# Kernel optimization log

Hardware: AMD Instinct MI355X
Metric: run time of the kernel (lower is better)

The kernel has to match this reference:

```python
import jax, jax.numpy as jnp
import numpy as np
import math

N = 100000
E = 1600000
D_IN = 128
H = 128
OUT = 10
NEG = -1e30


def setup_inputs() -> dict:
    key = jax.random.key(0)
    ks = jax.random.split(key, 24)
    def lin(k, fi, fo):
        s = 1.0 / np.sqrt(fi)
        return jax.random.uniform(k, (fi, fo), jnp.float32, -s, s)
    inp = {
        'x': jax.random.normal(ks[0], (N, D_IN), jnp.float32),
        'edge_index': jax.random.randint(ks[1], (2, E), 0, N, jnp.int64),
        'W1': lin(ks[2], D_IN, H), 'b1': jnp.zeros((H,), jnp.float32),
        'ws1': lin(ks[3], H, 1), 'bs1': jnp.zeros((1,), jnp.float32),
        'W2': lin(ks[4], H, H), 'b2': jnp.zeros((H,), jnp.float32),
        'ws2': lin(ks[5], H, 1), 'bs2': jnp.zeros((1,), jnp.float32),
        'W3': lin(ks[6], H, H), 'b3': jnp.zeros((H,), jnp.float32),
        'ws3': lin(ks[7], H, 1), 'bs3': jnp.zeros((1,), jnp.float32),
        'M1': lin(ks[8], 2 * H, H), 'bm1': jnp.zeros((H,), jnp.float32),
        'M2': lin(ks[9], H, H // 2), 'bm2': jnp.zeros((H // 2,), jnp.float32),
        'M3': lin(ks[10], H // 2, OUT), 'bm3': jnp.zeros((OUT,), jnp.float32),
    }
    return inp


def _gcn(x, W, b, src, dst, node_mask, edge_mask):
    # GCNConv with self-loops: deg[i] = self_loop + in_degree over valid edges
    deg = node_mask + jax.ops.segment_sum(edge_mask, dst, num_segments=N)
    dinv = jnp.where(deg > 0, jax.lax.rsqrt(deg), 0.0)
    coef = edge_mask * dinv[src] * dinv[dst]            # [E]
    agg = jax.ops.segment_sum(coef[:, None] * x[src], dst, num_segments=N)
    agg = agg + (node_mask * dinv * dinv)[:, None] * x   # self-loop term
    return (agg @ W + b) * node_mask[:, None]


def _sag_pool(x, ws, bs, src, dst, node_mask, edge_mask, k):
    # score via 1-dim GCNConv, top-k (ratio 0.5) select, tanh gating, edge filtering
    score = _gcn(x, ws, bs, src, dst, node_mask, edge_mask)[:, 0]
    _, idx = jax.lax.top_k(jnp.where(node_mask > 0, score, -jnp.inf), k)
    new_mask = jnp.zeros((N,), x.dtype).at[idx].set(1.0)
    x_new = x * jnp.tanh(score)[:, None] * new_mask[:, None]
    e_new = edge_mask * new_mask[src] * new_mask[dst]
    return x_new, new_mask, e_new


def _readout(x, mask, k):
    mean = jnp.sum(x * mask[:, None], axis=0) / k
    mx = jnp.max(jnp.where(mask[:, None] > 0, x, NEG), axis=0)
    return jnp.concatenate([mean, mx])[None, :]   # [1, 2H]


def reference(x, edge_index, W1, b1, ws1, bs1, W2, b2, ws2, bs2, W3, b3, ws3, bs3, M1, bm1, M2, bm2, M3, bm3):
    src, dst = edge_index[0], edge_index[1]
    nm0 = jnp.ones((N,), jnp.float32)
    em0 = jnp.ones((E,), jnp.float32)
    k1 = math.ceil(0.5 * N)
    k2 = math.ceil(0.5 * k1)
    k3 = math.ceil(0.5 * k2)

    h1 = jax.nn.relu(_gcn(x, W1, b1, src, dst, nm0, em0))
    x1, nm1, em1 = _sag_pool(h1, ws1, bs1, src, dst, nm0, em0, k1)
    r1 = _readout(x1, nm1, k1)

    h2 = jax.nn.relu(_gcn(x1, W2, b2, src, dst, nm1, em1))
    x2, nm2, em2 = _sag_pool(h2, ws2, bs2, src, dst, nm1, em1, k2)
    r2 = _readout(x2, nm2, k2)

    h3 = jax.nn.relu(_gcn(x2, W3, b3, src, dst, nm2, em2))
    x3, nm3, em3 = _sag_pool(h3, ws3, bs3, src, dst, nm2, em2, k3)
    r3 = _readout(x3, nm3, k3)

    readout = r1 + r2 + r3                              # [1, 2H]
    y = jax.nn.relu(readout @ M1 + bm1)
    y = jax.nn.relu(y @ M2 + bm2)
    y = y @ M3 + bm3
    return jax.nn.log_softmax(y, axis=1)
```

## Files before the change

### kernel.cpp

```cpp
#include <hip/hip_runtime.h>
#include <cstdint>
#include <cstddef>

#define NN 100000
#define EE 1600000
#define HH 128
#define NB_N 391
#define NBKT 391
#define CAP 5120


static __device__ __forceinline__ unsigned fsort_(float f){
  unsigned u = __float_as_uint(f);
  return (u & 0x80000000u) ? ~u : (u | 0x80000000u);
}
static __device__ __forceinline__ unsigned bfbits_(float f){
  unsigned u = __float_as_uint(f);
  return (u + 0x7FFFu + ((u >> 16) & 1u)) >> 16;
}
static __device__ __forceinline__ unsigned bfpack_(float f0, float f1){
  return bfbits_(f0) | (bfbits_(f1) << 16);
}
static __device__ __forceinline__ float bflo_(unsigned u){ return __uint_as_float(u << 16); }
static __device__ __forceinline__ float bfhi_(unsigned u){ return __uint_as_float(u & 0xFFFF0000u); }

__global__ void k_edgeflag(const int* __restrict__ ei, unsigned* __restrict__ state,
                           unsigned* __restrict__ bktcnt){
  int t = threadIdx.x;
  if(t < 64){
    int v = ei[2*t + 1];
    unsigned long long m = __ballot(v != 0);
    if(t == 0) state[8] = (m == 0ull) ? 1u : 0u;
  }
  if(t >= 12 && t < 24) state[t] = 0u;
  for(int j=t; j<NBKT; j+=256) bktcnt[j] = 0u;
}

__global__ __launch_bounds__(256) void k_binA(const int* __restrict__ ei,
                     const unsigned* __restrict__ state,
                     unsigned* __restrict__ bktcnt, unsigned* __restrict__ staging){
  __shared__ unsigned lcnt[NBKT];
  __shared__ unsigned lloc[NBKT];
  int t = threadIdx.x;
  for(int j=t; j<NBKT; j+=256){ lcnt[j] = 0u; lloc[j] = 0u; }
  bool i64 = (state[8] != 0u);
  int e0 = blockIdx.x*4096;
  int es[16], ed[16];
  #pragma unroll
  for(int k=0;k<16;k++){
    int e = e0 + k*256 + t;
    int s = -1, d = 0;
    if(e < EE){
      if(i64){ s = ei[2*e]; d = ei[2*EE + 2*e]; }
      else   { s = ei[e];   d = ei[EE + e]; }
    }
    es[k] = s; ed[k] = d;
  }
  __syncthreads();
  #pragma unroll
  for(int k=0;k<16;k++){
    if(es[k] >= 0) atomicAdd(&lcnt[ed[k]>>8], 1u);
  }
  __syncthreads();
  for(int j=t; j<NBKT; j+=256){
    unsigned c = lcnt[j];
    lcnt[j] = c ? atomicAdd(&bktcnt[j], c) : 0u;
  }
  __syncthreads();
  #pragma unroll
  for(int k=0;k<16;k++){
    if(es[k] >= 0){
      int b = ed[k] >> 8;
      unsigned off = lcnt[b] + atomicAdd(&lloc[b], 1u);
      if(off < CAP)
        staging[(unsigned)b*CAP + off] = (unsigned)es[k] | (((unsigned)(ed[k] & 255)) << 17);
    }
  }
}

__global__ __launch_bounds__(256) void k_binB(const unsigned* __restrict__ staging,
                     const unsigned* __restrict__ bktcnt,
                     int* __restrict__ rs, int* __restrict__ rl, int* __restrict__ col,
                     float* __restrict__ dinv){
  __shared__ unsigned hist[256];
  __shared__ unsigned pref[256];
  __shared__ unsigned lfill[256];
  __shared__ unsigned baseSh;
  int t = threadIdx.x;
  int b = blockIdx.x;
  unsigned s = 0;
  for(int j=t; j<b; j+=256) s += bktcnt[j];
  pref[t] = s;
  __syncthreads();
  for(int off=128; off>0; off>>=1){
    if(t < off) pref[t] += pref[t+off];
    __syncthreads();
  }
  if(t == 0) baseSh = pref[0];
  __syncthreads();
  unsigned base = baseSh;
  unsigned cnt = bktcnt[b]; if(cnt > CAP) cnt = CAP;
  hist[t] = 0u; lfill[t] = 0u;
  __syncthreads();
  const unsigned* st = staging + (unsigned)b*CAP;
  for(unsigned i=t; i<cnt; i+=256) atomicAdd(&hist[st[i]>>17], 1u);
  __syncthreads();
  unsigned h = hist[t];
  pref[t] = h;
  __syncthreads();
  for(int off=1; off<256; off<<=1){
    unsigned u = (t >= off) ? pref[t-off] : 0u;
    __syncthreads();
    pref[t] += u;
    __syncthreads();
  }
  unsigned excl = pref[t] - h;
  int node = b*256 + t;
  if(node < NN){
    rs[node] = (int)(base + excl);
    rl[node] = (int)h;
    dinv[node] = rsqrtf(1.f + (float)h);
  }
  __syncthreads();
  pref[t] = excl;
  __syncthreads();
  for(unsigned i=t; i<cnt; i+=256){
    unsigned w = st[i];
    unsigned dl = w >> 17;
    unsigned pos = base + pref[dl] + atomicAdd(&lfill[dl], 1u);
    col[pos] = (int)(w & 0x1FFFFu);
  }
}

template<int MODE>
__global__ __launch_bounds__(256) void k_gemm(const void* __restrict__ xin_,
        const float* __restrict__ gate, const int* __restrict__ alist, int nrows,
        const float* __restrict__ W, unsigned short* __restrict__ y16){
  __shared__ float sX[16][68];
  __shared__ float sW[16][64];
  __shared__ int rowid[64];
  __shared__ float rowg[64];
  int row0 = blockIdx.x*64, col0 = blockIdx.y*64;
  int t = threadIdx.x;
  if(t < 64){
    int gr = row0 + t;
    int node = -1; float gg = 0.f;
    if(gr < nrows){
      node = MODE ? alist[gr] : gr;
      gg = MODE ? gate[node] : 1.f;
    }
    rowid[t] = node; rowg[t] = gg;
  }
  __syncthreads();
  int tx = t & 15, ty = t >> 4;
  float acc[4][4] = {{0.f}};
  const float* xf = (const float*)xin_;
  const unsigned short* xh = (const unsigned short*)xin_;
  for(int kb=0; kb<HH; kb+=16){
    #pragma unroll
    for(int j=0;j<4;j++){
      int r = (t>>4) + j*16;
      int k = t & 15;
      int node = rowid[r];
      float v = 0.f;
      if(node >= 0){
        if(MODE) v = __uint_as_float(((unsigned)xh[(size_t)node*HH + kb + k]) << 16) * rowg[r];
        else     v = xf[(size_t)node*HH + kb + k];
      }
      sX[k][r] = v;
    }
    #pragma unroll
    for(int j=0;j<4;j++){
      int k = (t>>6) + j*4;
      int c = t & 63;
      sW[k][c] = W[(size_t)(kb+k)*HH + col0 + c];
    }
    __syncthreads();
    #pragma unroll
    for(int k=0;k<16;k++){
      float4 xv = *(const float4*)&sX[k][ty*4];
      float4 wv = *(const float4*)&sW[k][tx*4];
      float xs[4] = {xv.x, xv.y, xv.z, xv.w};
      float wsv[4] = {wv.x, wv.y, wv.z, wv.w};
      #pragma unroll
      for(int a=0;a<4;a++)
        #pragma unroll
        for(int b=0;b<4;b++)
          acc[a][b] += xs[a]*wsv[b];
    }
    __syncthreads();
  }
  #pragma unroll
  for(int a=0;a<4;a++){
    int node = rowid[ty*4 + a];
    if(node >= 0){
      uint2 o;
      o.x = bfpack_(acc[a][0], acc[a][1]);
      o.y = bfpack_(acc[a][2], acc[a][3]);
      *(uint2*)&y16[(size_t)node*HH + col0 + tx*4] = o;
    }
  }
}

template<int LIST>
__global__ __launch_bounds__(256) void k_agg(const unsigned short* __restrict__ y16,
        const float* __restrict__ dinv,
        const int* __restrict__ rs, const int* __restrict__ rl,
        const int* __restrict__ col, const int* __restrict__ alist,
        const float* __restrict__ bias, const float* __restrict__ wsc,
        unsigned short* __restrict__ h16, float* __restrict__ p,
        unsigned* __restrict__ hist){
  if(blockIdx.x < 512) hist[blockIdx.x*256 + threadIdx.x] = 0u;
  int w = (blockIdx.x*256 + threadIdx.x) >> 6;
  int lane = threadIdx.x & 63;
  int g = lane >> 4, c = lane & 15;
  int node = LIST ? alist[w] : w;
  float di = dinv[node];
  int e0 = rs[node], len = rl[node];
  float a0=0,a1=0,a2=0,a3=0,a4=0,a5=0,a6=0,a7=0;
  int i = g;
  for(; i + 4 < len; i += 8){
    int s0 = col[e0+i], s1 = col[e0+i+4];
    float d0 = dinv[s0], d1 = dinv[s1];
    uint4 v0 = ((const uint4*)(y16 + (size_t)s0*HH))[c];
    uint4 v1 = ((const uint4*)(y16 + (size_t)s1*HH))[c];
    a0 += d0*bflo_(v0.x) + d1*bflo_(v1.x);
    a1 += d0*bfhi_(v0.x) + d1*bfhi_(v1.x);
    a2 += d0*bflo_(v0.y) + d1*bflo_(v1.y);
    a3 += d0*bfhi_(v0.y) + d1*bfhi_(v1.y);
    a4 += d0*bflo_(v0.z) + d1*bflo_(v1.z);
    a5 += d0*bfhi_(v0.z) + d1*bfhi_(v1.z);
    a6 += d0*bflo_(v0.w) + d1*bflo_(v1.w);
    a7 += d0*bfhi_(v0.w) + d1*bfhi_(v1.w);
  }
  if(i < len){
    int s = col[e0+i];
    float ds = dinv[s];
    uint4 v = ((const uint4*)(y16 + (size_t)s*HH))[c];
    a0 += ds*bflo_(v.x); a1 += ds*bfhi_(v.x);
    a2 += ds*bflo_(v.y); a3 += ds*bfhi_(v.y);
    a4 += ds*bflo_(v.z); a5 += ds*bfhi_(v.z);
    a6 += ds*bflo_(v.w); a7 += ds*bfhi_(v.w);
  }
  a0 += __shfl_xor(a0,16,64); a0 += __shfl_xor(a0,32,64);
  a1 += __shfl_xor(a1,16,64); a1 += __shfl_xor(a1,32,64);
  a2 += __shfl_xor(a2,16,64); a2 += __shfl_xor(a2,32,64);
  a3 += __shfl_xor(a3,16,64); a3 += __shfl_xor(a3,32,64);
  a4 += __shfl_xor(a4,16,64); a4 += __shfl_xor(a4,32,64);
  a5 += __shfl_xor(a5,16,64); a5 += __shfl_xor(a5,32,64);
  a6 += __shfl_xor(a6,16,64); a6 += __shfl_xor(a6,32,64);
  a7 += __shfl_xor(a7,16,64); a7 += __shfl_xor(a7,32,64);
  uint4 sv = ((const uint4*)(y16 + (size_t)node*HH))[c];
  const float4* b4 = (const float4*)bias;
  float4 bb0 = b4[2*c], bb1 = b4[2*c+1];
  float d2 = di*di;
  float o0 = fmaxf(di*a0 + d2*bflo_(sv.x) + bb0.x, 0.f);
  float o1 = fmaxf(di*a1 + d2*bfhi_(sv.x) + bb0.y, 0.f);
  float o2 = fmaxf(di*a2 + d2*bflo_(sv.y) + bb0.z, 0.f);
  float o3 = fmaxf(di*a3 + d2*bfhi_(sv.y) + bb0.w, 0.f);
  float o4 = fmaxf(di*a4 + d2*bflo_(sv.z) + bb1.x, 0.f);
  float o5 = fmaxf(di*a5 + d2*bfhi_(sv.z) + bb1.y, 0.f);
  float o6 = fmaxf(di*a6 + d2*bflo_(sv.w) + bb1.z, 0.f);
  float o7 = fmaxf(di*a7 + d2*bfhi_(sv.w) + bb1.w, 0.f);
  if(g == 0){
    uint4 o;
    o.x = bfpack_(o0,o1); o.y = bfpack_(o2,o3);
    o.z = bfpack_(o4,o5); o.w = bfpack_(o6,o7);
    ((uint4*)(h16 + (size_t)node*HH))[c] = o;
  }
  const float4* w4 = (const float4*)wsc;
  float4 w0 = w4[2*c], w1 = w4[2*c+1];
  float pp = o0*w0.x + o1*w0.y + o2*w0.z + o3*w0.w
           + o4*w1.x + o5*w1.y + o6*w1.z + o7*w1.w;
  pp += __shfl_xor(pp, 1, 64);
  pp += __shfl_xor(pp, 2, 64);
  pp += __shfl_xor(pp, 4, 64);
  pp += __shfl_xor(pp, 8, 64);
  if(lane == 0) p[node] = pp;
}

template<int LIST>
__global__ void k_score(const float* __restrict__ p, const float* __restrict__ dinv,
                        const int* __restrict__ rs, const int* __restrict__ rl,
                        const int* __restrict__ col, const int* __restrict__ alist, int n,
                        const float* __restrict__ bs, float* __restrict__ score,
                        unsigned* __restrict__ key, unsigned* __restrict__ hist){
  int w = blockIdx.x*256 + threadIdx.x;
  if(w >= n) return;
  int i = LIST ? alist[w] : w;
  float di = dinv[i];
  float s = 0.f;
  int e0 = rs[i], len = rl[i];
  for(int e=e0; e<e0+len; e++){
    int cidx = col[e];
    s += dinv[cidx]*p[cidx];
  }
  float sc = di*s + di*di*p[i] + bs[0];
  score[i] = sc;
  unsigned kv = fsort_(sc);
  key[i] = kv;
  atomicAdd(&hist[kv>>16], 1u);
}

__global__ void k_hist_lo(const unsigned* __restrict__ key, const unsigned* __restrict__ state,
                          unsigned* __restrict__ histB){
  int i = blockIdx.x*256 + threadIdx.x;
  if(i < NN){
    unsigned kv = key[i];
    if((kv >> 16) == state[0]) atomicAdd(&histB[kv & 0xFFFFu], 1u);
  }
}
__global__ void k_pick(const unsigned* __restrict__ hist, unsigned* __restrict__ state,
                       int k_in, int mode){
  __shared__ unsigned csum[256];
  int t = threadIdx.x;
  const uint4* h4 = (const uint4*)(hist + t*256);
  unsigned s = 0;
  for(int j=0;j<64;j++){ uint4 v = h4[j]; s += v.x+v.y+v.z+v.w; }
  csum[t] = s;
  __syncthreads();
  for(int off=1; off<256; off<<=1){
    unsigned v = (t+off < 256) ? csum[t+off] : 0u;
    __syncthreads();
    csum[t] += v;
    __syncthreads();
  }
  unsigned k = (mode == 0) ? (unsigned)k_in : state[1];
  unsigned above = csum[t] - s;
  if(above < k && above + s >= k){
    unsigned run = above;
    for(int j=255; j>=0; j--){
      unsigned c = hist[t*256+j];
      if(run + c >= k){
        if(mode == 0){ state[0] = (unsigned)(t*256+j); state[1] = k - run; }
        else { state[2] = (state[0] << 16) | (unsigned)(t*256+j); state[3] = k - run; }
        break;
      }
      run += c;
    }
  }
}

__global__ __launch_bounds__(256) void k_maskCR(unsigned* __restrict__ key,
        const float* __restrict__ score, const unsigned* __restrict__ state,
        const unsigned short* __restrict__ h16,
        unsigned char* __restrict__ selm, float* __restrict__ gate,
        int* __restrict__ alist_out, unsigned* __restrict__ acounter,
        float* __restrict__ rpart, int slotbase){
  __shared__ int wcnt[4];
  __shared__ int priorSh;
  __shared__ int redi[256];
  __shared__ float gl[256];
  __shared__ unsigned char slf[256];
  __shared__ float4 red[256];
  __shared__ float out2[256];
  int t = threadIdx.x;
  int i = blockIdx.x*256 + t;
  unsigned T = state[2];
  int trem = (int)state[3];
  unsigned kv = (i < NN) ? key[i] : 0u;
  bool match = (kv == T);
  unsigned long long m = __ballot(match);
  int lane = t & 63, wid = t >> 6;
  if(lane == 0) wcnt[wid] = __popcll(m);
  if(t == 0) priorSh = 0;
  __syncthreads();
  int hasMatch = wcnt[0] | wcnt[1] | wcnt[2] | wcnt[3];
  int bbase = blockIdx.x*256;
  if(hasMatch){
    int cm = 0;
    for(int j = t*4; j < bbase; j += 1024){
      uint4 kk = *(const uint4*)&key[j];
      cm += (kk.x==T) + (kk.y==T) + (kk.z==T) + (kk.w==T);
    }
    redi[t] = cm;
    __syncthreads();
    for(int off=128; off>0; off>>=1){
      if(t < off) redi[t] += redi[t+off];
      __syncthreads();
    }
    if(t == 0) priorSh = redi[0];
    __syncthreads();
  }
  int pre = 0;
  for(int w=0; w<wid; w++) pre += wcnt[w];
  int lrank = __popcll(m & ((1ull << lane) - 1ull));
  int rank = priorSh + pre + lrank;
  bool sel = (kv > T) || (match && rank < trem);
  float gg = sel ? tanhf(score[i]) : 0.f;
  gl[t] = gg;
  slf[t] = sel ? 1 : 0;
  if(i < NN){
    selm[i] = sel ? 1 : 0;
    gate[i] = gg;
    if(!sel) key[i] = 0u;
  }
  unsigned long long sm = __ballot(sel);
  unsigned abase = 0;
  if(lane == 0) abase = atomicAdd(acounter, (unsigned)__popcll(sm));
  abase = (unsigned)__shfl((int)abase, 0, 64);
  if(sel) alist_out[abase + __popcll(sm & ((1ull << lane) - 1ull))] = i;
  __syncthreads();
  int ch = t & 15;
  int slot = t >> 4;
  float mm[8] = {0,0,0,0,0,0,0,0};
  float MM[8] = {-1e30f,-1e30f,-1e30f,-1e30f,-1e30f,-1e30f,-1e30f,-1e30f};
  for(int itr=0; itr<16; itr++){
    int nl = slot + itr*16;
    int node = bbase + nl;
    if(node < NN && slf[nl]){
      float g = gl[nl];
      uint4 v = ((const uint4*)(h16 + (size_t)node*HH))[ch];
      float x0 = g*bflo_(v.x), x1 = g*bfhi_(v.x);
      float x2 = g*bflo_(v.y), x3 = g*bfhi_(v.y);
      float x4 = g*bflo_(v.z), x5 = g*bfhi_(v.z);
      float x6 = g*bflo_(v.w), x7 = g*bfhi_(v.w);
      mm[0]+=x0; mm[1]+=x1; mm[2]+=x2; mm[3]+=x3;
      mm[4]+=x4; mm[5]+=x5; mm[6]+=x6; mm[7]+=x7;
      MM[0]=fmaxf(MM[0],x0); MM[1]=fmaxf(MM[1],x1); MM[2]=fmaxf(MM[2],x2); MM[3]=fmaxf(MM[3],x3);
      MM[4]=fmaxf(MM[4],x4); MM[5]=fmaxf(MM[5],x5); MM[6]=fmaxf(MM[6],x6); MM[7]=fmaxf(MM[7],x7);
    }
  }
  #pragma unroll
  for(int half=0; half<2; half++){
    red[t] = make_float4(mm[half*4+0],mm[half*4+1],mm[half*4+2],mm[half*4+3]);
    __syncthreads();
    if(t < 16){
      float4 sacc = red[t];
      for(int j=1;j<16;j++){
        float4 o = red[t + 16*j];
        sacc.x += o.x; sacc.y += o.y; sacc.z += o.z; sacc.w += o.w;
      }
      int d = t*8 + half*4;
      out2[d+0] = sacc.x; out2[d+1] = sacc.y; out2[d+2] = sacc.z; out2[d+3] = sacc.w;
    }
    __syncthreads();
    red[t] = make_float4(MM[half*4+0],MM[half*4+1],MM[half*4+2],MM[half*4+3]);
    __syncthreads();
    if(t < 16){
      float4 sacc = red[t];
      for(int j=1;j<16;j++){
        float4 o = red[t + 16*j];
        sacc.x = fmaxf(sacc.x,o.x); sacc.y = fmaxf(sacc.y,o.y);
        sacc.z = fmaxf(sacc.z,o.z); sacc.w = fmaxf(sacc.w,o.w);
      }
      int d = 128 + t*8 + half*4;
      out2[d+0] = sacc.x; out2[d+1] = sacc.y; out2[d+2] = sacc.z; out2[d+3] = sacc.w;
    }
    __syncthreads();
  }
  rpart[(size_t)(slotbase + blockIdx.x)*256 + t] = out2[t];
}

__global__ __launch_bounds__(256) void k_compact(const int* __restrict__ alist, int n,
        const unsigned char* __restrict__ selm,
        const int* __restrict__ rs_old, const int* __restrict__ rl_old,
        const int* __restrict__ col_old,
        int* __restrict__ rs_new, int* __restrict__ rl_new, int* __restrict__ col_new,
        float* __restrict__ dinv, unsigned* __restrict__ ecnt){
  __shared__ unsigned gcnt[16];
  __shared__ unsigned gbase[16];
  __shared__ unsigned blkbase;
  int t = threadIdx.x;
  int g = t >> 4, lane = t & 15;
  int gsh = ((t >> 4) & 3) * 16;
  int idx = blockIdx.x*16 + g;
  int node = -1, e0 = 0, len = 0;
  if(idx < n){ node = alist[idx]; e0 = rs_old[node]; len = rl_old[node]; }
  int cnt = 0;
  for(int i=lane; i<len; i+=16) cnt += selm[col_old[e0+i]];
  cnt += __shfl_xor(cnt,1,64); cnt += __shfl_xor(cnt,2,64);
  cnt += __shfl_xor(cnt,4,64); cnt += __shfl_xor(cnt,8,64);
  if(lane == 0) gcnt[g] = (node >= 0) ? (unsigned)cnt : 0u;
  __syncthreads();
  if(t == 0){
    unsigned s = 0;
    for(int j=0;j<16;j++){ gbase[j] = s; s += gcnt[j]; }
    blkbase = s ? atomicAdd(ecnt, s) : 0u;
  }
  __syncthreads();
  unsigned base = blkbase + gbase[g];
  if(node >= 0 && lane == 0){
    rs_new[node] = (int)base;
    rl_new[node] = cnt;
    dinv[node] = rsqrtf(1.f + (float)cnt);
  }
  int pos = (int)base;
  for(int i0=0; i0<len; i0+=16){
    int i = i0 + lane;
    bool keep = false; int s = 0;
    if(i < len){ s = col_old[e0+i]; keep = (selm[s] != 0); }
    unsigned long long b = __ballot(keep);
    unsigned gb = (unsigned)((b >> gsh) & 0xFFFFull);
    int rank = __popc(gb & ((1u << lane) - 1u));
    if(keep) col_new[pos + rank] = s;
    pos += __popc(gb);
  }
}

__global__ void k_mlp(const float* __restrict__ rpart,
                      const float* __restrict__ M1, const float* __restrict__ bm1,
                      const float* __restrict__ M2, const float* __restrict__ bm2,
                      const float* __restrict__ M3, const float* __restrict__ bm3,
                      float* __restrict__ out){
  __shared__ float R[256];
  __shared__ float y1[128];
  __shared__ float y2[64];
  __shared__ float y3[16];
  int t = threadIdx.x;
  const float kinv[3] = {1.f/50000.f, 1.f/25000.f, 1.f/12500.f};
  if(t < 128){
    float acc = 0.f;
    for(int l=0; l<3; l++){
      float s0=0.f,s1=0.f,s2=0.f,s3=0.f;
      int base = l*NB_N;
      int j = 0;
      for(; j+3 < NB_N; j += 4){
        s0 += rpart[(size_t)(base+j  )*256 + t];
        s1 += rpart[(size_t)(base+j+1)*256 + t];
        s2 += rpart[(size_t)(base+j+2)*256 + t];
        s3 += rpart[(size_t)(base+j+3)*256 + t];
      }
      for(; j < NB_N; j++) s0 += rpart[(size_t)(base+j)*256 + t];
      acc += ((s0+s1)+(s2+s3)) * kinv[l];
    }
    R[t] = acc;
  } else {
    float acc = 0.f;
    for(int l=0; l<3; l++){
      float m0=-1e30f,m1=-1e30f,m2=-1e30f,m3=-1e30f;
      int base = l*NB_N;
      int j = 0;
      for(; j+3 < NB_N; j += 4){
        m0 = fmaxf(m0, rpart[(size_t)(base+j  )*256 + t]);
        m1 = fmaxf(m1, rpart[(size_t)(base+j+1)*256 + t]);
        m2 = fmaxf(m2, rpart[(size_t)(base+j+2)*256 + t]);
        m3 = fmaxf(m3, rpart[(size_t)(base+j+3)*256 + t]);
      }
      for(; j < NB_N; j++) m0 = fmaxf(m0, rpart[(size_t)(base+j)*256 + t]);
      acc += fmaxf(fmaxf(m0,m1), fmaxf(m2,m3));
    }
    R[t] = acc;
  }
  __syncthreads();
  if(t < 128){
    float a = bm1[t];
    for(int d=0; d<256; d++) a += R[d]*M1[d*128+t];
    y1[t] = fmaxf(a, 0.f);
  }
  __syncthreads();
  if(t < 64){
    float a = bm2[t];
    for(int d=0; d<128; d++) a += y1[d]*M2[d*64+t];
    y2[t] = fmaxf(a, 0.f);
  }
  __syncthreads();
  if(t < 10){
    float a = bm3[t];
    for(int d=0; d<64; d++) a += y2[d]*M3[d*10+t];
    y3[t] = a;
  }
  __syncthreads();
  if(t == 0){
    float mx = -1e30f;
    for(int o=0;o<10;o++) mx = fmaxf(mx, y3[o]);
    float s = 0.f;
    for(int o=0;o<10;o++) s += expf(y3[o]-mx);
    float ls = logf(s);
    for(int o=0;o<10;o++) out[o] = y3[o] - mx - ls;
  }
}

extern "C" void kernel_launch(void* const* d_in, const int* in_sizes, int n_in,
                              void* d_out, int out_size, void* d_ws, size_t ws_size,
                              hipStream_t stream){
  (void)in_sizes; (void)n_in; (void)out_size; (void)ws_size;
  const float* x  = (const float*)d_in[0];
  const int*   ei = (const int*)d_in[1];
  const float* W[3]   = {(const float*)d_in[2],  (const float*)d_in[6],  (const float*)d_in[10]};
  const float* bb[3]  = {(const float*)d_in[3],  (const float*)d_in[7],  (const float*)d_in[11]};
  const float* wsc[3] = {(const float*)d_in[4],  (const float*)d_in[8],  (const float*)d_in[12]};
  const float* bsc[3] = {(const float*)d_in[5],  (const float*)d_in[9],  (const float*)d_in[13]};
  const float* M1  = (const float*)d_in[14];
  const float* bm1 = (const float*)d_in[15];
  const float* M2  = (const float*)d_in[16];
  const float* bm2 = (const float*)d_in[17];
  const float* M3  = (const float*)d_in[18];
  const float* bm3 = (const float*)d_in[19];
  float* out = (float*)d_out;

  char* base = (char*)d_ws;
  size_t off = 0;
  auto alloc = [&](size_t bytes)->char*{
    char* ptr = base + off;
    off += (bytes + 511) & ~(size_t)511;
    return ptr;
  };
  unsigned short* y16  = (unsigned short*)alloc((size_t)NN*HH*2);
  unsigned short* h16  = (unsigned short*)alloc((size_t)NN*HH*2);
  int*      col0      = (int*)     alloc((size_t)EE*4);
  int*      col1      = (int*)     alloc((size_t)EE*4);
  int*      col2      = (int*)     alloc((size_t)EE*4);
  unsigned* staging   = (unsigned*)alloc((size_t)NBKT*CAP*4);
  int*      rs0       = (int*)     alloc((size_t)NN*4);
  int*      rl0       = (int*)     alloc((size_t)NN*4);
  int*      rs1       = (int*)     alloc((size_t)NN*4);
  int*      rl1       = (int*)     alloc((size_t)NN*4);
  int*      rs2       = (int*)     alloc((size_t)NN*4);
  int*      rl2       = (int*)     alloc((size_t)NN*4);
  float*    dinv      = (float*)   alloc((size_t)NN*4);
  float*    pbuf      = (float*)   alloc((size_t)NN*4);
  float*    score     = (float*)   alloc((size_t)NN*4);
  float*    gate      = (float*)   alloc((size_t)NN*4);
  unsigned* key       = (unsigned*)alloc((size_t)NN*4);
  unsigned char* selm = (unsigned char*)alloc((size_t)NN);
  int*      alistA    = (int*)     alloc((size_t)50000*4);
  int*      alistB    = (int*)     alloc((size_t)25000*4);
  unsigned* hist      = (unsigned*)alloc((size_t)2*65536*4);
  unsigned* bktcnt    = (unsigned*)alloc((size_t)(NBKT+1)*4);
  unsigned* state     = (unsigned*)alloc(256);
  float*    rpart     = (float*)   alloc((size_t)3*NB_N*256*4);

  k_edgeflag<<<1,256,0,stream>>>(ei, state, bktcnt);
  k_binA<<<NBKT,256,0,stream>>>(ei, state, bktcnt, staging);
  k_binB<<<NBKT,256,0,stream>>>(staging, bktcnt, rs0, rl0, col0, dinv);

  k_gemm<0><<<dim3(1563,2),256,0,stream>>>(x, nullptr, nullptr, NN, W[0], y16);
  k_agg<0><<<25000,256,0,stream>>>(y16, dinv, rs0, rl0, col0, nullptr, bb[0], wsc[0], h16, pbuf, hist);
  k_score<0><<<NB_N,256,0,stream>>>(pbuf, dinv, rs0, rl0, col0, nullptr, NN, bsc[0], score, key, hist);
  k_pick<<<1,256,0,stream>>>(hist, state, 50000, 0);
  k_hist_lo<<<NB_N,256,0,stream>>>(key, state, hist + 65536);
  k_pick<<<1,256,0,stream>>>(hist + 65536, state, 0, 1);
  k_maskCR<<<NB_N,256,0,stream>>>(key, score, state, h16, selm, gate, alistA, state+12, rpart, 0);
  k_compact<<<3125,256,0,stream>>>(alistA, 50000, selm, rs0, rl0, col0, rs1, rl1, col1, dinv, state+16);

  k_gemm<1><<<dim3(782,2),256,0,stream>>>(h16, gate, alistA, 50000, W[1], y16);
  k_agg<1><<<12500,256,0,stream>>>(y16, dinv, rs1, rl1, col1, alistA, bb[1], wsc[1], h16, pbuf, hist);
  k_score<1><<<196,256,0,stream>>>(pbuf, dinv, rs1, rl1, col1, alistA, 50000, bsc[1], score, key, hist);
  k_pick<<<1,256,0,stream>>>(hist, state, 25000, 0);
  k_hist_lo<<<NB_N,256,0,stream>>>(key, state, hist + 65536);
  k_pick<<<1,256,0,stream>>>(hist + 65536, state, 0, 1);
  k_maskCR<<<NB_N,256,0,stream>>>(key, score, state, h16, selm, gate, alistB, state+13, rpart, NB_N);
  k_compact<<<1563,256,0,stream>>>(alistB, 25000, selm, rs1, rl1, col1, rs2, rl2, col2, dinv, state+17);

  k_gemm<1><<<dim3(391,2),256,0,stream>>>(h16, gate, alistB, 25000, W[2], y16);
  k_agg<1><<<6250,256,0,stream>>>(y16, dinv, rs2, rl2, col2, alistB, bb[2], wsc[2], h16, pbuf, hist);
  k_score<1><<<98,256,0,stream>>>(pbuf, dinv, rs2, rl2, col2, alistB, 25000, bsc[2], score, key, hist);
  k_pick<<<1,256,0,stream>>>(hist, state, 12500, 0);
  k_hist_lo<<<NB_N,256,0,stream>>>(key, state, hist + 65536);
  k_pick<<<1,256,0,stream>>>(hist + 65536, state, 0, 1);
  k_maskCR<<<NB_N,256,0,stream>>>(key, score, state, h16, selm, gate, alistA, state+14, rpart, 2*NB_N);

  k_mlp<<<1,256,0,stream>>>(rpart, M1, bm1, M2, bm2, M3, bm3, out);
}
```

Baseline: 802.9 us.

## Fuse top-k threshold search into one single-block radix-select kernel

Replaces the pick / low-histogram / pick sequence with one single-block kernel. After the global high-16-bit histogram it runs two 8-bit refinement passes over all keys using shared-memory histograms. This cuts two launches per pooling stage and halves the histogram buffer. The key-zeroing for unselected nodes moves from k_maskCR into k_compact. In exchange, one block now scans 100k keys twice serially, which could cost more than the launches it removes.

Result: slower. 943.1 us (+17.5%).

```diff
diff --git a/kernel.cpp b/kernel.cpp
--- a/kernel.cpp
+++ b/kernel.cpp
@@ -210,7 +210,7 @@
         const float* __restrict__ bias, const float* __restrict__ wsc,
         unsigned short* __restrict__ h16, float* __restrict__ p,
         unsigned* __restrict__ hist){
-  if(blockIdx.x < 512) hist[blockIdx.x*256 + threadIdx.x] = 0u;
+  if(blockIdx.x < 256) hist[blockIdx.x*256 + threadIdx.x] = 0u;
   int w = (blockIdx.x*256 + threadIdx.x) >> 6;
   int lane = threadIdx.x & 63;
   int g = lane >> 4, c = lane & 15;
@@ -302,46 +302,79 @@
   atomicAdd(&hist[kv>>16], 1u);
 }
 
-__global__ void k_hist_lo(const unsigned* __restrict__ key, const unsigned* __restrict__ state,
-                          unsigned* __restrict__ histB){
-  int i = blockIdx.x*256 + threadIdx.x;
-  if(i < NN){
-    unsigned kv = key[i];
-    if((kv >> 16) == state[0]) atomicAdd(&histB[kv & 0xFFFFu], 1u);
-  }
-}
-__global__ void k_pick(const unsigned* __restrict__ hist, unsigned* __restrict__ state,
-                       int k_in, int mode){
+__global__ __launch_bounds__(256) void k_thresh(const unsigned* __restrict__ key,
+        const unsigned* __restrict__ hist, unsigned* __restrict__ state, int k_in){
   __shared__ unsigned csum[256];
-  int t = threadIdx.x;
-  const uint4* h4 = (const uint4*)(hist + t*256);
-  unsigned s = 0;
-  for(int j=0;j<64;j++){ uint4 v = h4[j]; s += v.x+v.y+v.z+v.w; }
-  csum[t] = s;
-  __syncthreads();
-  for(int off=1; off<256; off<<=1){
-    unsigned v = (t+off < 256) ? csum[t+off] : 0u;
-    __syncthreads();
-    csum[t] += v;
-    __syncthreads();
-  }
-  unsigned k = (mode == 0) ? (unsigned)k_in : state[1];
-  unsigned above = csum[t] - s;
-  if(above < k && above + s >= k){
-    unsigned run = above;
+  __shared__ unsigned lh[256];
+  __shared__ unsigned selB, selR;
+  int t = threadIdx.x;
+  {
+    const uint4* h4 = (const uint4*)(hist + t*256);
+    unsigned s = 0;
+    for(int j=0;j<64;j++){ uint4 v = h4[j]; s += v.x+v.y+v.z+v.w; }
+    csum[t] = s;
+    __syncthreads();
+    for(int off=1; off<256; off<<=1){
+      unsigned v = (t+off < 256) ? csum[t+off] : 0u;
+      __syncthreads();
+      csum[t] += v;
+      __syncthreads();
+    }
+    unsigned k = (unsigned)k_in;
+    unsigned above = csum[t] - s;
+    if(above < k && above + s >= k){
+      unsigned run = above;
+      for(int j=255; j>=0; j--){
+        unsigned c = hist[t*256+j];
+        if(run + c >= k){ selB = (unsigned)(t*256+j); selR = k - run; break; }
+        run += c;
+      }
+    }
+    __syncthreads();
+  }
+  unsigned hi = selB, k = selR;
+  lh[t] = 0u;
+  __syncthreads();
+  for(int i=t; i<NN/4; i+=256){
+    uint4 kk = ((const uint4*)key)[i];
+    if((kk.x>>16) == hi) atomicAdd(&lh[(kk.x>>8)&255], 1u);
+    if((kk.y>>16) == hi) atomicAdd(&lh[(kk.y>>8)&255], 1u);
+    if((kk.z>>16) == hi) atomicAdd(&lh[(kk.z>>8)&255], 1u);
+    if((kk.w>>16) == hi) atomicAdd(&lh[(kk.w>>8)&255], 1u);
+  }
+  __syncthreads();
+  if(t == 0){
+    unsigned run = 0;
     for(int j=255; j>=0; j--){
-      unsigned c = hist[t*256+j];
-      if(run + c >= k){
-        if(mode == 0){ state[0] = (unsigned)(t*256+j); state[1] = k - run; }
-        else { state[2] = (state[0] << 16) | (unsigned)(t*256+j); state[3] = k - run; }
-        break;
-      }
+      unsigned c = lh[j];
+      if(run + c >= k){ selB = (unsigned)j; selR = k - run; break; }
       run += c;
     }
   }
-}
-
-__global__ __launch_bounds__(256) void k_maskCR(unsigned* __restrict__ key,
+  __syncthreads();
+  unsigned pfx = (hi << 8) | selB;
+  k = selR;
+  lh[t] = 0u;
+  __syncthreads();
+  for(int i=t; i<NN/4; i+=256){
+    uint4 kk = ((const uint4*)key)[i];
+    if((kk.x>>8) == pfx) atomicAdd(&lh[kk.x&255], 1u);
+    if((kk.y>>8) == pfx) atomicAdd(&lh[kk.y&255], 1u);
+    if((kk.z>>8) == pfx) atomicAdd(&lh[kk.z&255], 1u);
+    if((kk.w>>8) == pfx) atomicAdd(&lh[kk.w&255], 1u);
+  }
+  __syncthreads();
+  if(t == 0){
+    unsigned run = 0;
+    for(int j=255; j>=0; j--){
+      unsigned c = lh[j];
+      if(run + c >= k){ state[2] = (pfx << 8) | (unsigned)j; state[3] = k - run; break; }
+      run += c;
+    }
+  }
+}
+
+__global__ __launch_bounds__(256) void k_maskCR(const unsigned* __restrict__ key,
         const float* __restrict__ score, const unsigned* __restrict__ state,
         const unsigned short* __restrict__ h16,
         unsigned char* __restrict__ selm, float* __restrict__ gate,
@@ -393,7 +426,6 @@
   if(i < NN){
     selm[i] = sel ? 1 : 0;
     gate[i] = gg;
-    if(!sel) key[i] = 0u;
   }
   unsigned long long sm = __ballot(sel);
   unsigned abase = 0;
@@ -453,7 +485,7 @@
 }
 
 __global__ __launch_bounds__(256) void k_compact(const int* __restrict__ alist, int n,
-        const unsigned char* __restrict__ selm,
+        const unsigned char* __restrict__ selm, unsigned* __restrict__ key,
         const int* __restrict__ rs_old, const int* __restrict__ rl_old,
         const int* __restrict__ col_old,
         int* __restrict__ rs_new, int* __restrict__ rl_new, int* __restrict__ col_new,
@@ -462,6 +494,8 @@
   __shared__ unsigned gbase[16];
   __shared__ unsigned blkbase;
   int t = threadIdx.x;
+  for(int i = blockIdx.x*256 + t; i < NN; i += gridDim.x*256)
+    if(!selm[i]) key[i] = 0u;
   int g = t >> 4, lane = t & 15;
   int gsh = ((t >> 4) & 3) * 16;
   int idx = blockIdx.x*16 + g;
@@ -616,7 +650,7 @@
   unsigned char* selm = (unsigned char*)alloc((size_t)NN);
   int*      alistA    = (int*)     alloc((size_t)50000*4);
   int*      alistB    = (int*)     alloc((size_t)25000*4);
-  unsigned* hist      = (unsigned*)alloc((size_t)2*65536*4);
+  unsigned* hist      = (unsigned*)alloc((size_t)65536*4);
   unsigned* bktcnt    = (unsigned*)alloc((size_t)(NBKT+1)*4);
   unsigned* state     = (unsigned*)alloc(256);
   float*    rpart     = (float*)   alloc((size_t)3*NB_N*256*4);
@@ -628,27 +662,21 @@
   k_gemm<0><<<dim3(1563,2),256,0,stream>>>(x, nullptr, nullptr, NN, W[0], y16);
   k_agg<0><<<25000,256,0,stream>>>(y16, dinv, rs0, rl0, col0, nullptr, bb[0], wsc[0], h16, pbuf, hist);
   k_score<0><<<NB_N,256,0,stream>>>(pbuf, dinv, rs0, rl0, col0, nullptr, NN, bsc[0], score, key, hist);
-  k_pick<<<1,256,0,stream>>>(hist, state, 50000, 0);
-  k_hist_lo<<<NB_N,256,0,stream>>>(key, state, hist + 65536);
-  k_pick<<<1,256,0,stream>>>(hist + 65536, state, 0, 1);
+  k_thresh<<<1,256,0,stream>>>(key, hist, state, 50000);
   k_maskCR<<<NB_N,256,0,stream>>>(key, score, state, h16, selm, gate, alistA, state+12, rpart, 0);
-  k_compact<<<3125,256,0,stream>>>(alistA, 50000, selm, rs0, rl0, col0, rs1, rl1, col1, dinv, state+16);
+  k_compact<<<3125,256,0,stream>>>(alistA, 50000, selm, key, rs0, rl0, col0, rs1, rl1, col1, dinv, state+16);
 
   k_gemm<1><<<dim3(782,2),256,0,stream>>>(h16, gate, alistA, 50000, W[1], y16);
   k_agg<1><<<12500,256,0,stream>>>(y16, dinv, rs1, rl1, col1, alistA, bb[1], wsc[1], h16, pbuf, hist);
   k_score<1><<<196,256,0,stream>>>(pbuf, dinv, rs1, rl1, col1, alistA, 50000, bsc[1], score, key, hist);
-  k_pick<<<1,256,0,stream>>>(hist, state, 25000, 0);
-  k_hist_lo<<<NB_N,256,0,stream>>>(key, state, hist + 65536);
-  k_pick<<<1,256,0,stream>>>(hist + 65536, state, 0, 1);
+  k_thresh<<<1,256,0,stream>>>(key, hist, state, 25000);
   k_maskCR<<<NB_N,256,0,stream>>>(key, score, state, h16, selm, gate, alistB, state+13, rpart, NB_N);
-  k_compact<<<1563,256,0,stream>>>(alistB, 25000, selm, rs1, rl1, col1, rs2, rl2, col2, dinv, state+17);
+  k_compact<<<1563,256,0,stream>>>(alistB, 25000, selm, key, rs1, rl1, col1, rs2, rl2, col2, dinv, state+17);
 
   k_gemm<1><<<dim3(391,2),256,0,stream>>>(h16, gate, alistB, 25000, W[2], y16);
   k_agg<1><<<6250,256,0,stream>>>(y16, dinv, rs2, rl2, col2, alistB, bb[2], wsc[2], h16, pbuf, hist);
   k_score<1><<<98,256,0,stream>>>(pbuf, dinv, rs2, rl2, col2, alistB, 25000, bsc[2], score, key, hist);
-  k_pick<<<1,256,0,stream>>>(hist, state, 12500, 0);
-  k_hist_lo<<<NB_N,256,0,stream>>>(key, state, hist + 65536);
-  k_pick<<<1,256,0,stream>>>(hist + 65536, state, 0, 1);
+  k_thresh<<<1,256,0,stream>>>(key, hist, state, 12500);
   k_maskCR<<<NB_N,256,0,stream>>>(key, score, state, h16, selm, gate, alistA, state+14, rpart, 2*NB_N);
 
   k_mlp<<<1,256,0,stream>>>(rpart, M1, bm1, M2, bm2, M3, bm3, out);
```
